# Optimization experiments

Measured on AMD Instinct MI355X. Metric: run time of the kernel, lower is better.

The kernel has to match this reference:

```python
import jax, jax.numpy as jnp
import numpy as np

B, T, C = 4, 1024, 1024
L, H = 4, 8
D = C // H          # head_size = 128
F = 4 * C           # ff_hd = 4096
EPS = 1e-5          # torch LayerNorm default


def _ln(x, s, b):
    m = jnp.mean(x, axis=-1, keepdims=True)
    v = jnp.var(x, axis=-1, keepdims=True)
    return (x - m) * jax.lax.rsqrt(v + EPS) * s + b


def setup_inputs() -> dict:
    key = jax.random.key(0)
    ks = jax.random.split(key, 16)
    std = 0.02
    return {
        "x": jax.random.normal(ks[0], (B, T, C), jnp.float32),
        "pos_emb": jax.random.normal(ks[1], (T, C), jnp.float32) * std,
        # per-head QKV projections, stacked over layers: [L, H, C, D]
        "Wq": jax.random.normal(ks[2], (L, H, C, D), jnp.float32) * std,
        "Wk": jax.random.normal(ks[3], (L, H, C, D), jnp.float32) * std,
        "Wv": jax.random.normal(ks[4], (L, H, C, D), jnp.float32) * std,
        "Wo": jax.random.normal(ks[5], (L, C, C), jnp.float32) * std,
        "bo": jnp.zeros((L, C), jnp.float32),
        "ln1_s": jnp.ones((L, C), jnp.float32),
        "ln1_b": jnp.zeros((L, C), jnp.float32),
        "ln2_s": jnp.ones((L, C), jnp.float32),
        "ln2_b": jnp.zeros((L, C), jnp.float32),
        "W1": jax.random.normal(ks[6], (L, C, F), jnp.float32) * std,
        "b1": jnp.zeros((L, F), jnp.float32),
        "W2": jax.random.normal(ks[7], (L, F, C), jnp.float32) * std,
        "b2": jnp.zeros((L, C), jnp.float32),
        "lnf_s": jnp.ones((C,), jnp.float32),
        "lnf_b": jnp.zeros((C,), jnp.float32),
    }


def _encoder(x, pos_emb, Wq, Wk, Wv, Wo, bo, ln1_s, ln1_b, ln2_s, ln2_b,
             W1, b1, W2, b2, lnf_s, lnf_b):
    x = x + pos_emb  # [B,T,C]
    scale = D ** -0.5

    def step(h_x, p):
        (wq, wk, wv, wo, bo_, l1s, l1b, l2s, l2b, w1, b1_, w2, b2_) = p
        xn = _ln(h_x, l1s, l1b)
        q = jnp.einsum('btc,hcd->bhtd', xn, wq)
        k = jnp.einsum('btc,hcd->bhtd', xn, wk)
        v = jnp.einsum('btc,hcd->bhtd', xn, wv)
        att = jax.nn.softmax(jnp.einsum('bhtd,bhsd->bhts', q, k) * scale, axis=-1)
        o = jnp.einsum('bhts,bhsd->bhtd', att, v)          # [B,H,T,D]
        o = o.transpose(0, 2, 1, 3).reshape(B, T, C)        # concat heads
        h_x = h_x + o @ wo + bo_
        xn2 = _ln(h_x, l2s, l2b)
        h_x = h_x + jax.nn.relu(xn2 @ w1 + b1_) @ w2 + b2_
        # att returned as [H,B,T,T] to mirror per-head list ordering
        return h_x, att.transpose(1, 0, 2, 3)

    x, atts = jax.lax.scan(step, x, (Wq, Wk, Wv, Wo, bo, ln1_s, ln1_b,
                                     ln2_s, ln2_b, W1, b1, W2, b2))
    x = _ln(x, lnf_s, lnf_b)
    return x, atts  # atts: [L, H, B, T, T]


def reference(x, pos_emb, Wq, Wk, Wv, Wo, bo, ln1_s, ln1_b, ln2_s, ln2_b,
              W1, b1, W2, b2, lnf_s, lnf_b):
    return _encoder(x, pos_emb, Wq, Wk, Wv, Wo, bo, ln1_s, ln1_b, ln2_s, ln2_b,
                    W1, b1, W2, b2, lnf_s, lnf_b)
```

## Files before the change

kernel.cpp:

```cpp
#include <hip/hip_runtime.h>
#include <hip/hip_bf16.h>

typedef __attribute__((ext_vector_type(8))) short bf16x8;
typedef __attribute__((ext_vector_type(4))) float f32x4;
typedef __hip_bfloat16 bf16;

__global__ __launch_bounds__(256) void transpose_cvt(
    const float* __restrict__ in, bf16* __restrict__ out, int R, int Cc)
{
  __shared__ float tile[32][33];
  long base = (long)blockIdx.z * R * Cc;
  int c0 = blockIdx.x * 32, r0 = blockIdx.y * 32;
  int tx = threadIdx.x & 31, ty = threadIdx.x >> 5;
  #pragma unroll
  for (int i = 0; i < 32; i += 8)
    tile[ty + i][tx] = in[base + (long)(r0 + ty + i) * Cc + (c0 + tx)];
  __syncthreads();
  #pragma unroll
  for (int i = 0; i < 32; i += 8)
    out[base + (long)(c0 + ty + i) * R + (r0 + tx)] =
        __float2bfloat16(tile[tx][ty + i]);
}

__global__ __launch_bounds__(256) void add_pos(
    const float* __restrict__ x, const float* __restrict__ pos,
    float* __restrict__ h)
{
  int i = blockIdx.x * 1024 + threadIdx.x;
  #pragma unroll
  for (int j = 0; j < 4; ++j) {
    int idx = i + j * 256;
    h[idx] = x[idx] + pos[idx & ((1 << 20) - 1)];
  }
}

__device__ inline float wave_sum(float v) {
  #pragma unroll
  for (int o = 32; o; o >>= 1) v += __shfl_down(v, o, 64);
  return v;
}

template<bool F32OUT>
__global__ __launch_bounds__(256) void layernorm_k(
    const float* __restrict__ x, const float* __restrict__ s,
    const float* __restrict__ b, void* __restrict__ outv)
{
  __shared__ float red[8];
  long row = blockIdx.x;
  const float* xr = x + (row << 10);
  int t = threadIdx.x;
  float v[4]; float sum = 0.f, sq = 0.f;
  #pragma unroll
  for (int i = 0; i < 4; ++i) {
    v[i] = xr[t + i * 256];
    sum += v[i]; sq += v[i] * v[i];
  }
  sum = wave_sum(sum); sq = wave_sum(sq);
  if ((t & 63) == 0) { red[t >> 6] = sum; red[4 + (t >> 6)] = sq; }
  __syncthreads();
  sum = red[0] + red[1] + red[2] + red[3];
  sq  = red[4] + red[5] + red[6] + red[7];
  float mean = sum * (1.f / 1024.f);
  float var  = sq * (1.f / 1024.f) - mean * mean;
  float rstd = rsqrtf(var + 1e-5f);
  #pragma unroll
  for (int i = 0; i < 4; ++i) {
    int c = t + i * 256;
    float y = (v[i] - mean) * rstd * s[c] + b[c];
    if (F32OUT) ((float*)outv)[(row << 10) + c] = y;
    else        ((bf16*)outv)[(row << 10) + c] = __float2bfloat16(y);
  }
}

__global__ __launch_bounds__(256) void softmax_attn(
    float* __restrict__ att, bf16* __restrict__ attb)
{
  __shared__ float red[8];
  long r = blockIdx.x;
  float* ar = att + (r << 10);
  int t = threadIdx.x;
  float v[4]; float mx = -3.4e38f;
  #pragma unroll
  for (int i = 0; i < 4; ++i) { v[i] = ar[t + i * 256]; mx = fmaxf(mx, v[i]); }
  #pragma unroll
  for (int o = 32; o; o >>= 1) mx = fmaxf(mx, __shfl_down(mx, o, 64));
  if ((t & 63) == 0) red[t >> 6] = mx;
  __syncthreads();
  mx = fmaxf(fmaxf(red[0], red[1]), fmaxf(red[2], red[3]));
  float sum = 0.f;
  #pragma unroll
  for (int i = 0; i < 4; ++i) { v[i] = __expf(v[i] - mx); sum += v[i]; }
  sum = wave_sum(sum);
  if ((t & 63) == 0) red[4 + (t >> 6)] = sum;
  __syncthreads();
  sum = red[4] + red[5] + red[6] + red[7];
  float inv = 1.f / sum;
  int hh = (int)(r >> 12) & 7;
  int bb = (int)(r >> 10) & 3;
  long tt = r & 1023;
  bf16* abr = attb + ((((long)(bb * 8 + hh) << 10) + tt) << 10);
  #pragma unroll
  for (int i = 0; i < 4; ++i) {
    float p = v[i] * inv;
    ar[t + i * 256]  = p;
    abr[t + i * 256] = __float2bfloat16(p);
  }
}

enum { EPI_BHTD = 0, EPI_VT, EPI_SCORES, EPI_ATTV, EPI_RES, EPI_RELU };

template<int EPI>
__global__ __launch_bounds__(256, 2) void gemm_bt(
    const bf16* __restrict__ A, const bf16* __restrict__ Bt,
    void* __restrict__ Cout, const float* __restrict__ bias, float scale,
    int M, int N, int K, int lda, int ldb, long sAb, long sBb)
{
  __shared__ __align__(16) bf16 sA[128 * 64];
  __shared__ __align__(16) bf16 sB[128 * 64];
  const int tid = threadIdx.x;
  const int bn = blockIdx.x, bm = blockIdx.y, bz = blockIdx.z;
  const bf16* Ab = A + bz * sAb + (long)bm * 128 * lda;
  const bf16* Bb = Bt + bz * sBb + (long)bn * 128 * ldb;
  const int wave = tid >> 6, lane = tid & 63;
  const int wm = (wave >> 1) * 64, wn = (wave & 1) * 64;
  const int quad = lane >> 4, l16 = lane & 15;

  f32x4 acc[4][4] = {};

  for (int k0 = 0; k0 < K; k0 += 64) {
    #pragma unroll
    for (int i = 0; i < 4; ++i) {
      int c = i * 256 + tid;
      int row = c >> 3, col = (c & 7) << 3;
      int ldsoff = (i * 256 + (tid & ~63)) << 3;
      __builtin_amdgcn_global_load_lds(
          (const __attribute__((address_space(1))) void*)(Ab + (long)row * lda + (k0 + col)),
          (__attribute__((address_space(3))) void*)(sA + ldsoff), 16, 0, 0);
      __builtin_amdgcn_global_load_lds(
          (const __attribute__((address_space(1))) void*)(Bb + (long)row * ldb + (k0 + col)),
          (__attribute__((address_space(3))) void*)(sB + ldsoff), 16, 0, 0);
    }
    __syncthreads();
    #pragma unroll
    for (int kk = 0; kk < 64; kk += 32) {
      bf16x8 af[4], bfr[4];
      #pragma unroll
      for (int i = 0; i < 4; ++i) {
        af[i]  = *(const bf16x8*)(sA + (wm + i * 16 + l16) * 64 + kk + quad * 8);
        bfr[i] = *(const bf16x8*)(sB + (wn + i * 16 + l16) * 64 + kk + quad * 8);
      }
      #pragma unroll
      for (int i = 0; i < 4; ++i)
        #pragma unroll
        for (int j = 0; j < 4; ++j)
          acc[i][j] = __builtin_amdgcn_mfma_f32_16x16x32_bf16(
              af[i], bfr[j], acc[i][j], 0, 0, 0);
    }
    __syncthreads();
  }

  #pragma unroll
  for (int i = 0; i < 4; ++i) {
    #pragma unroll
    for (int j = 0; j < 4; ++j) {
      #pragma unroll
      for (int r = 0; r < 4; ++r) {
        int m = (bm << 7) + wm + i * 16 + (quad << 2) + r;
        int n = (bn << 7) + wn + j * 16 + l16;
        float v = acc[i][j][r];
        if (EPI == EPI_BHTD) {
          long idx = ((long)((m >> 10) * 8 + (n >> 7)) << 17) +
                     ((long)(m & 1023) << 7) + (n & 127);
          ((bf16*)Cout)[idx] = __float2bfloat16(v);
        } else if (EPI == EPI_VT) {
          long idx = ((long)((m >> 10) * 8 + (n >> 7)) << 17) +
                     ((long)(n & 127) << 10) + (m & 1023);
          ((bf16*)Cout)[idx] = __float2bfloat16(v);
        } else if (EPI == EPI_SCORES) {
          long idx = ((long)((bz & 7) * 4 + (bz >> 3)) << 20) +
                     ((long)m << 10) + n;
          ((float*)Cout)[idx] = v * scale;
        } else if (EPI == EPI_ATTV) {
          long idx = ((long)(bz >> 3) << 20) + ((long)m << 10) +
                     ((bz & 7) << 7) + n;
          ((bf16*)Cout)[idx] = __float2bfloat16(v);
        } else if (EPI == EPI_RES) {
          long idx = (long)m * N + n;
          ((float*)Cout)[idx] += v + bias[n];
        } else {
          long idx = (long)m * N + n;
          ((bf16*)Cout)[idx] = __float2bfloat16(fmaxf(v + bias[n], 0.f));
        }
      }
    }
  }
}

extern "C" void kernel_launch(void* const* d_in, const int* in_sizes, int n_in,
                              void* d_out, int out_size, void* d_ws, size_t ws_size,
                              hipStream_t stream)
{
  const float* x     = (const float*)d_in[0];
  const float* pos   = (const float*)d_in[1];
  const float* Wq    = (const float*)d_in[2];
  const float* Wk    = (const float*)d_in[3];
  const float* Wv    = (const float*)d_in[4];
  const float* Wo    = (const float*)d_in[5];
  const float* bo    = (const float*)d_in[6];
  const float* ln1_s = (const float*)d_in[7];
  const float* ln1_b = (const float*)d_in[8];
  const float* ln2_s = (const float*)d_in[9];
  const float* ln2_b = (const float*)d_in[10];
  const float* W1    = (const float*)d_in[11];
  const float* b1    = (const float*)d_in[12];
  const float* W2    = (const float*)d_in[13];
  const float* b2    = (const float*)d_in[14];
  const float* lnf_s = (const float*)d_in[15];
  const float* lnf_b = (const float*)d_in[16];
  float* out = (float*)d_out;

  char* w = (char*)d_ws;
  float* h  = (float*)w;
  bf16* xn  = (bf16*)(w + (16l  << 20));
  bf16* q   = (bf16*)(w + (24l  << 20));
  bf16* kb  = (bf16*)(w + (32l  << 20));
  bf16* vT  = (bf16*)(w + (40l  << 20));
  bf16* o   = (bf16*)(w + (48l  << 20));
  bf16* big = (bf16*)(w + (56l  << 20));
  bf16* WqT = (bf16*)(w + (120l << 20));
  bf16* WkT = (bf16*)(w + (128l << 20));
  bf16* WvT = (bf16*)(w + (136l << 20));
  bf16* WoT = (bf16*)(w + (144l << 20));
  bf16* W1T = (bf16*)(w + (152l << 20));
  bf16* W2T = (bf16*)(w + (184l << 20));

  dim3 blk(256);
  transpose_cvt<<<dim3(4, 32, 32),  blk, 0, stream>>>(Wq, WqT, 1024, 128);
  transpose_cvt<<<dim3(4, 32, 32),  blk, 0, stream>>>(Wk, WkT, 1024, 128);
  transpose_cvt<<<dim3(4, 32, 32),  blk, 0, stream>>>(Wv, WvT, 1024, 128);
  transpose_cvt<<<dim3(32, 32, 4),  blk, 0, stream>>>(Wo, WoT, 1024, 1024);
  transpose_cvt<<<dim3(128, 32, 4), blk, 0, stream>>>(W1, W1T, 1024, 4096);
  transpose_cvt<<<dim3(32, 128, 4), blk, 0, stream>>>(W2, W2T, 4096, 1024);

  add_pos<<<4096, blk, 0, stream>>>(x, pos, h);

  const float scale = 0.08838834764831845f;
  for (int l = 0; l < 4; ++l) {
    layernorm_k<false><<<4096, blk, 0, stream>>>(h, ln1_s + l * 1024, ln1_b + l * 1024, xn);
    gemm_bt<EPI_BHTD><<<dim3(8, 32, 1), blk, 0, stream>>>(
        xn, WqT + (long)l * 1048576, q, nullptr, 0.f, 4096, 1024, 1024, 1024, 1024, 0, 0);
    gemm_bt<EPI_BHTD><<<dim3(8, 32, 1), blk, 0, stream>>>(
        xn, WkT + (long)l * 1048576, kb, nullptr, 0.f, 4096, 1024, 1024, 1024, 1024, 0, 0);
    gemm_bt<EPI_VT><<<dim3(8, 32, 1), blk, 0, stream>>>(
        xn, WvT + (long)l * 1048576, vT, nullptr, 0.f, 4096, 1024, 1024, 1024, 1024, 0, 0);

    float* attL = out + 4194304l + (long)l * 33554432l;
    gemm_bt<EPI_SCORES><<<dim3(8, 8, 32), blk, 0, stream>>>(
        q, kb, attL, nullptr, scale, 1024, 1024, 128, 128, 128, 131072l, 131072l);
    softmax_attn<<<32768, blk, 0, stream>>>(attL, big);
    gemm_bt<EPI_ATTV><<<dim3(1, 8, 32), blk, 0, stream>>>(
        big, vT, o, nullptr, 0.f, 1024, 128, 1024, 1024, 1024, 1048576l, 131072l);
    gemm_bt<EPI_RES><<<dim3(8, 32, 1), blk, 0, stream>>>(
        o, WoT + (long)l * 1048576, h, bo + l * 1024, 0.f, 4096, 1024, 1024, 1024, 1024, 0, 0);

    layernorm_k<false><<<4096, blk, 0, stream>>>(h, ln2_s + l * 1024, ln2_b + l * 1024, xn);
    gemm_bt<EPI_RELU><<<dim3(32, 32, 1), blk, 0, stream>>>(
        xn, W1T + (long)l * 4194304, big, b1 + l * 4096, 0.f, 4096, 4096, 1024, 1024, 1024, 0, 0);
    gemm_bt<EPI_RES><<<dim3(8, 32, 1), blk, 0, stream>>>(
        big, W2T + (long)l * 4194304, h, b2 + l * 1024, 0.f, 4096, 1024, 4096, 4096, 4096, 0, 0);
  }
  layernorm_k<true><<<4096, blk, 0, stream>>>(h, lnf_s, lnf_b, out);
}
```

Measured before the change: 2.374 ms.

## Fuse attention scores, softmax and P·V into one kernel

Replaces the separate QK^T GEMM, row-softmax kernel and attention-times-V GEMM with a single kernel per 64-query tile that computes the full 1024-wide score rows in registers, does a block-wide softmax via LDS reductions, writes fp32 probabilities once, and keeps bf16 probabilities in LDS for the P·V MFMA. This removes the fp32 score write plus read-back, the bf16 probability round-trip through global memory, and two kernel launches per layer. In exchange, the kernel uses about 132KB of LDS and heavy register pressure (128 accumulator floats per lane), which limits occupancy, and K/V operands are read directly from global memory without LDS staging.

```diff
diff --git a/kernel.cpp b/kernel.cpp
--- a/kernel.cpp
+++ b/kernel.cpp
@@ -72,39 +72,159 @@
   }
 }
 
-__global__ __launch_bounds__(256) void softmax_attn(
-    float* __restrict__ att, bf16* __restrict__ attb)
-{
-  __shared__ float red[8];
-  long r = blockIdx.x;
-  float* ar = att + (r << 10);
-  int t = threadIdx.x;
-  float v[4]; float mx = -3.4e38f;
-  #pragma unroll
-  for (int i = 0; i < 4; ++i) { v[i] = ar[t + i * 256]; mx = fmaxf(mx, v[i]); }
-  #pragma unroll
-  for (int o = 32; o; o >>= 1) mx = fmaxf(mx, __shfl_down(mx, o, 64));
-  if ((t & 63) == 0) red[t >> 6] = mx;
-  __syncthreads();
-  mx = fmaxf(fmaxf(red[0], red[1]), fmaxf(red[2], red[3]));
-  float sum = 0.f;
-  #pragma unroll
-  for (int i = 0; i < 4; ++i) { v[i] = __expf(v[i] - mx); sum += v[i]; }
-  sum = wave_sum(sum);
-  if ((t & 63) == 0) red[4 + (t >> 6)] = sum;
-  __syncthreads();
-  sum = red[4] + red[5] + red[6] + red[7];
-  float inv = 1.f / sum;
-  int hh = (int)(r >> 12) & 7;
-  int bb = (int)(r >> 10) & 3;
-  long tt = r & 1023;
-  bf16* abr = attb + ((((long)(bb * 8 + hh) << 10) + tt) << 10);
-  #pragma unroll
-  for (int i = 0; i < 4; ++i) {
-    float p = v[i] * inv;
-    ar[t + i * 256]  = p;
-    abr[t + i * 256] = __float2bfloat16(p);
-  }
+__global__ __launch_bounds__(512, 2) void fused_attn(
+    const bf16* __restrict__ q, const bf16* __restrict__ kb,
+    const bf16* __restrict__ vT, float* __restrict__ attL,
+    bf16* __restrict__ o)
+{
+  __shared__ __align__(16) bf16 p_lds[64 * 1032];
+  __shared__ float red[2][8][64];
+  const int tid  = threadIdx.x;
+  const int wave = tid >> 6, lane = tid & 63;
+  const int quad = lane >> 4, l16 = lane & 15;
+  const int bm = blockIdx.x, bz = blockIdx.y;
+  const int b = bz >> 3, hh = bz & 7;
+  const bf16* qb  = q  + ((long)bz << 17) + ((long)bm << 13);
+  const bf16* kbz = kb + ((long)bz << 17);
+  const bf16* vbz = vT + ((long)bz << 17);
+  const int wn = wave << 7;
+
+  f32x4 acc[4][8] = {};
+  #pragma unroll
+  for (int kk = 0; kk < 4; ++kk) {
+    bf16x8 af[4];
+    #pragma unroll
+    for (int i = 0; i < 4; ++i)
+      af[i] = *(const bf16x8*)(qb + (i * 16 + l16) * 128 + kk * 32 + quad * 8);
+    #pragma unroll
+    for (int jg = 0; jg < 8; jg += 4) {
+      bf16x8 bfr[4];
+      #pragma unroll
+      for (int j = 0; j < 4; ++j)
+        bfr[j] = *(const bf16x8*)(kbz +
+            (long)(wn + (jg + j) * 16 + l16) * 128 + kk * 32 + quad * 8);
+      #pragma unroll
+      for (int j = 0; j < 4; ++j)
+        #pragma unroll
+        for (int i = 0; i < 4; ++i)
+          acc[i][jg + j] = __builtin_amdgcn_mfma_f32_16x16x32_bf16(
+              af[i], bfr[j], acc[i][jg + j], 0, 0, 0);
+    }
+  }
+
+  float mx[4][4];
+  #pragma unroll
+  for (int i = 0; i < 4; ++i)
+    #pragma unroll
+    for (int r = 0; r < 4; ++r) {
+      float m = -3.4e38f;
+      #pragma unroll
+      for (int j = 0; j < 8; ++j) m = fmaxf(m, acc[i][j][r]);
+      #pragma unroll
+      for (int off = 1; off < 16; off <<= 1) m = fmaxf(m, __shfl_xor(m, off, 64));
+      mx[i][r] = m;
+    }
+  if (l16 == 0) {
+    #pragma unroll
+    for (int i = 0; i < 4; ++i)
+      #pragma unroll
+      for (int r = 0; r < 4; ++r)
+        red[0][wave][i * 16 + quad * 4 + r] = mx[i][r];
+  }
+  __syncthreads();
+  #pragma unroll
+  for (int i = 0; i < 4; ++i)
+    #pragma unroll
+    for (int r = 0; r < 4; ++r) {
+      int row = i * 16 + quad * 4 + r;
+      float m = red[0][0][row];
+      #pragma unroll
+      for (int w = 1; w < 8; ++w) m = fmaxf(m, red[0][w][row]);
+      mx[i][r] = m;
+    }
+
+  const float scale = 0.08838834764831845f;
+  float inv[4][4];
+  #pragma unroll
+  for (int i = 0; i < 4; ++i)
+    #pragma unroll
+    for (int r = 0; r < 4; ++r) {
+      float s = 0.f;
+      #pragma unroll
+      for (int j = 0; j < 8; ++j) {
+        float e = __expf((acc[i][j][r] - mx[i][r]) * scale);
+        acc[i][j][r] = e; s += e;
+      }
+      #pragma unroll
+      for (int off = 1; off < 16; off <<= 1) s += __shfl_xor(s, off, 64);
+      inv[i][r] = s;
+    }
+  if (l16 == 0) {
+    #pragma unroll
+    for (int i = 0; i < 4; ++i)
+      #pragma unroll
+      for (int r = 0; r < 4; ++r)
+        red[1][wave][i * 16 + quad * 4 + r] = inv[i][r];
+  }
+  __syncthreads();
+  #pragma unroll
+  for (int i = 0; i < 4; ++i)
+    #pragma unroll
+    for (int r = 0; r < 4; ++r) {
+      int row = i * 16 + quad * 4 + r;
+      float s = 0.f;
+      #pragma unroll
+      for (int w = 0; w < 8; ++w) s += red[1][w][row];
+      inv[i][r] = 1.f / s;
+    }
+
+  long ob = ((long)(hh * 4 + b) << 20) + ((long)(bm * 64) << 10);
+  #pragma unroll
+  for (int i = 0; i < 4; ++i)
+    #pragma unroll
+    for (int r = 0; r < 4; ++r) {
+      int row = i * 16 + quad * 4 + r;
+      float iv = inv[i][r];
+      #pragma unroll
+      for (int j = 0; j < 8; ++j) {
+        float p = acc[i][j][r] * iv;
+        int col = wn + j * 16 + l16;
+        attL[ob + ((long)row << 10) + col] = p;
+        p_lds[row * 1032 + col] = __float2bfloat16(p);
+      }
+    }
+  __syncthreads();
+
+  const int wm2 = (wave >> 2) << 5;
+  const int wd  = (wave & 3) << 5;
+  f32x4 acc2[2][2] = {};
+  #pragma unroll 4
+  for (int s0 = 0; s0 < 1024; s0 += 32) {
+    bf16x8 pa[2], vv[2];
+    #pragma unroll
+    for (int i = 0; i < 2; ++i)
+      pa[i] = *(const bf16x8*)(p_lds + (wm2 + i * 16 + l16) * 1032 + s0 + quad * 8);
+    #pragma unroll
+    for (int j = 0; j < 2; ++j)
+      vv[j] = *(const bf16x8*)(vbz + (long)(wd + j * 16 + l16) * 1024 + s0 + quad * 8);
+    #pragma unroll
+    for (int i = 0; i < 2; ++i)
+      #pragma unroll
+      for (int j = 0; j < 2; ++j)
+        acc2[i][j] = __builtin_amdgcn_mfma_f32_16x16x32_bf16(
+            pa[i], vv[j], acc2[i][j], 0, 0, 0);
+  }
+  long ob2 = ((long)b << 20) + ((long)bm << 16) + (hh << 7);
+  #pragma unroll
+  for (int i = 0; i < 2; ++i)
+    #pragma unroll
+    for (int j = 0; j < 2; ++j)
+      #pragma unroll
+      for (int r = 0; r < 4; ++r) {
+        int t = wm2 + i * 16 + quad * 4 + r;
+        int d = wd + j * 16 + l16;
+        o[ob2 + ((long)t << 10) + d] = __float2bfloat16(acc2[i][j][r]);
+      }
 }
 
 enum { EPI_BHTD = 0, EPI_VT, EPI_SCORES, EPI_ATTV, EPI_RES, EPI_RELU };
@@ -244,7 +364,6 @@
 
   add_pos<<<4096, blk, 0, stream>>>(x, pos, h);
 
-  const float scale = 0.08838834764831845f;
   for (int l = 0; l < 4; ++l) {
     layernorm_k<false><<<4096, blk, 0, stream>>>(h, ln1_s + l * 1024, ln1_b + l * 1024, xn);
     gemm_bt<EPI_BHTD><<<dim3(8, 32, 1), blk, 0, stream>>>(
@@ -255,11 +374,8 @@
         xn, WvT + (long)l * 1048576, vT, nullptr, 0.f, 4096, 1024, 1024, 1024, 1024, 0, 0);
 
     float* attL = out + 4194304l + (long)l * 33554432l;
-    gemm_bt<EPI_SCORES><<<dim3(8, 8, 32), blk, 0, stream>>>(
-        q, kb, attL, nullptr, scale, 1024, 1024, 128, 128, 128, 131072l, 131072l);
-    softmax_attn<<<32768, blk, 0, stream>>>(attL, big);
-    gemm_bt<EPI_ATTV><<<dim3(1, 8, 32), blk, 0, stream>>>(
-        big, vT, o, nullptr, 0.f, 1024, 128, 1024, 1024, 1024, 1048576l, 131072l);
+    fused_attn<<<dim3(16, 32), dim3(512), 0, stream>>>(q, kb, vT, attL, o);
+
     gemm_bt<EPI_RES><<<dim3(8, 32, 1), blk, 0, stream>>>(
         o, WoT + (long)l * 1048576, h, bo + l * 1024, 0.f, 4096, 1024, 1024, 1024, 1024, 0, 0);
 
```

After: 2.262 ms. 1.05x faster.
